# Kernel optimization log

Hardware: AMD Instinct MI355X
Metric: run time of the kernel (lower is better)

## Reference

```python
import jax, jax.numpy as jnp
import numpy as np

N2, N1, N0 = 25000, 50000, 100000
E2, E1, E0 = 250000, 500000, 1000000
CIN, H, COUT = 64, 128, 64
BN_EPS = 1e-5


def setup_inputs() -> dict:
    key = jax.random.key(0)
    ks = jax.random.split(key, 26)
    inp = {
        'x': jax.random.normal(ks[0], (N2, CIN), jnp.float32),
        'edge_index': jax.random.randint(ks[1], (2, E2), 0, N2),
        'xs0': jax.random.normal(ks[2], (N0, H), jnp.float32),
        'xs1': jax.random.normal(ks[3], (N1, H), jnp.float32),
        'ei0': jax.random.randint(ks[4], (2, E0), 0, N0),
        'ei1': jax.random.randint(ks[5], (2, E1), 0, N1),
        'ew0': jax.random.uniform(ks[6], (E0,), jnp.float32, 0.1, 1.0),
        'ew1': jax.random.uniform(ks[7], (E1,), jnp.float32, 0.1, 1.0),
        # pooling perms: unique indices of kept nodes at the finer level
        'perm0': jax.random.permutation(ks[8], N0)[:N1],
        'perm1': jax.random.permutation(ks[9], N1)[:N2],
        # GIN layer 1: in=64 -> hidden//2=64 (MLP: Lin, ReLU, Lin), then BN
        'W1a': 0.1 * jax.random.normal(ks[10], (CIN, H // 2), jnp.float32),
        'b1a': jnp.zeros((H // 2,), jnp.float32),
        'W1b': 0.1 * jax.random.normal(ks[11], (H // 2, H // 2), jnp.float32),
        'b1b': jnp.zeros((H // 2,), jnp.float32),
        'g1': jnp.ones((H // 2,), jnp.float32),
        'bt1': jnp.zeros((H // 2,), jnp.float32),
        # GIN layer 2: 64 -> hidden=128
        'W2a': 0.1 * jax.random.normal(ks[12], (H // 2, H), jnp.float32),
        'b2a': jnp.zeros((H,), jnp.float32),
        'W2b': 0.1 * jax.random.normal(ks[13], (H, H), jnp.float32),
        'b2b': jnp.zeros((H,), jnp.float32),
        'g2': jnp.ones((H,), jnp.float32),
        'bt2': jnp.zeros((H,), jnp.float32),
        # GCN up_convs (improved=True): hidden->hidden, hidden->out
        'Wg0': 0.1 * jax.random.normal(ks[14], (H, H), jnp.float32),
        'bg0': jnp.zeros((H,), jnp.float32),
        'Wg1': 0.1 * jax.random.normal(ks[15], (H, COUT), jnp.float32),
        'bg1': jnp.zeros((COUT,), jnp.float32),
    }
    return inp


def _gin_layer(x, ei, Wa, ba, Wb, bb, g, bt):
    """GINConv (eps=0) + ReLU + BatchNorm1d (training-mode stats)."""
    n = x.shape[0]
    agg = jax.ops.segment_sum(x[ei[0]], ei[1], num_segments=n)
    h = x + agg  # (1 + eps) * x + sum of neighbors, eps = 0
    h = jnp.maximum(h @ Wa + ba, 0.0) @ Wb + bb  # MLP: Lin-ReLU-Lin
    h = jnp.maximum(h, 0.0)  # F.relu on conv output
    mu = h.mean(axis=0)
    var = jnp.mean((h - mu) ** 2, axis=0)  # biased var (BatchNorm1d)
    return g * (h - mu) * jax.lax.rsqrt(var + BN_EPS) + bt


def _gcn_improved(x, ei, ew, W, b):
    """GCNConv(improved=True): self-loop weight 2, symmetric norm."""
    n = x.shape[0]
    h = x @ W
    deg = jax.ops.segment_sum(ew, ei[1], num_segments=n) + 2.0  # +2I self loops
    dis = jax.lax.rsqrt(deg)
    norm = dis[ei[0]] * ew * dis[ei[1]]
    out = jax.ops.segment_sum(norm[:, None] * h[ei[0]], ei[1], num_segments=n)
    out = out + (2.0 * dis * dis)[:, None] * h  # self-loop contribution
    return out + b


def reference(x, edge_index, xs0, xs1, ei0, ei1, ew0, ew1, perm0, perm1,
              W1a, b1a, W1b, b1b, g1, bt1,
              W2a, b2a, W2b, b2b, g2, bt2,
              Wg0, bg0, Wg1, bg1):
    # projection convs on the coarsest graph
    h = _gin_layer(x, edge_index, W1a, b1a, W1b, b1b, g1, bt1)
    h = _gin_layer(h, edge_index, W2a, b2a, W2b, b2b, g2, bt2)
    # upsample step 1 (i=0, j=1): scatter into level-1 graph, GCN, ReLU
    up = jnp.zeros_like(xs1).at[perm1].set(h)
    h = jnp.maximum(_gcn_improved(up, ei1, ew1, Wg0, bg0), 0.0)
    # upsample step 2 (i=1, j=0): scatter into level-0 graph, final GCN
    up = jnp.zeros_like(xs0).at[perm0].set(h)
    return _gcn_improved(up, ei0, ew0, Wg1, bg1)
```

## Files before the change

kernel.cpp:

```cpp
#include <hip/hip_runtime.h>
#include <hip/hip_fp16.h>
#include <type_traits>

#define NN2 25000
#define NN1 50000
#define NN0 100000
#define EE2 250000
#define EE1 500000
#define EE0 1000000
#define NTOTC 175000
#define ETOTC 1750000
#define NB 684
#define CHUNK 4096
#define NBLK 428
#define BN_EPS 1e-5f

static inline int cdiv(long a, long b) { return (int)((a + b - 1) / b); }

typedef _Float16 half8 __attribute__((ext_vector_type(8)));
typedef float f32x4 __attribute__((ext_vector_type(4)));

template <int K, int M, bool RELU, bool BNIN, bool BNOUT, typename OT>
__global__ __launch_bounds__(256) void mfma_gemm_kernel(
    const __half* __restrict__ in, const float* __restrict__ W,
    const float* __restrict__ bias,
    const float* __restrict__ sums, const float* __restrict__ sumsq,
    const float* __restrict__ g, const float* __restrict__ bt,
    float* __restrict__ osum, float* __restrict__ osq,
    OT* __restrict__ out, int n)
{
    constexpr int BM = 64;
    constexpr int LDA = K + 8;
    constexpr int NC = M / 16;
    __shared__ __align__(16) _Float16 Ah[BM * LDA];
    __shared__ __align__(16) _Float16 Wt[M * LDA];
    const int tid = threadIdx.x;
    const int r0 = blockIdx.x * BM;

    for (int idx = tid; idx < K * M; idx += 256) {
        int k = idx / M, m = idx % M;
        Wt[m * LDA + k] = (_Float16)W[idx];
    }
    for (int idx = tid; idx < BM * K; idx += 256) {
        int r = idx / K, k = idx % K;
        int gr = r0 + r;
        float v = (gr < n) ? __half2float(in[(long)gr * K + k]) : 0.f;
        if (BNIN) {
            float mu = sums[k] * (1.f / NN2);
            float rs = rsqrtf(sumsq[k] * (1.f / NN2) - mu * mu + BN_EPS);
            v = g[k] * rs * (v - mu) + bt[k];
        }
        Ah[r * LDA + k] = (_Float16)v;
    }
    __syncthreads();

    const int wid = tid >> 6, lane = tid & 63;
    const int rw = wid * 16;
    const int arow = rw + (lane & 15);
    const int koff = (lane >> 4) * 8;

    f32x4 acc[NC];
    #pragma unroll
    for (int c = 0; c < NC; ++c) acc[c] = f32x4{0.f, 0.f, 0.f, 0.f};

    #pragma unroll
    for (int k0 = 0; k0 < K; k0 += 32) {
        half8 a = *(const half8*)&Ah[arow * LDA + k0 + koff];
        #pragma unroll
        for (int c = 0; c < NC; ++c) {
            half8 b = *(const half8*)&Wt[(c * 16 + (lane & 15)) * LDA + k0 + koff];
            acc[c] = __builtin_amdgcn_mfma_f32_16x16x32_f16(a, b, acc[c], 0, 0, 0);
        }
    }

    float* bs = (float*)Ah;
    if (BNOUT) {
        __syncthreads();
        if (tid < 2 * M) bs[tid] = 0.f;
        __syncthreads();
    }

    const int drow = r0 + rw + 4 * (lane >> 4);
    #pragma unroll
    for (int c = 0; c < NC; ++c) {
        int col = c * 16 + (lane & 15);
        float bv = (bias != nullptr) ? bias[col] : 0.f;
        float sc = 0.f, qc = 0.f;
        #pragma unroll
        for (int j = 0; j < 4; ++j) {
            int r = drow + j;
            if (r < n) {
                float v = acc[c][j] + bv;
                if (RELU) v = fmaxf(v, 0.f);
                if constexpr (std::is_same<OT, __half>::value)
                    out[(long)r * M + col] = __float2half(v);
                else
                    out[(long)r * M + col] = v;
                if (BNOUT) { sc += v; qc += v * v; }
            }
        }
        if (BNOUT) {
            atomicAdd(&bs[col], sc);
            atomicAdd(&bs[M + col], qc);
        }
    }
    if (BNOUT) {
        __syncthreads();
        if (tid < M) {
            atomicAdd(&osum[tid], bs[tid]);
            atomicAdd(&osq[tid], bs[M + tid]);
        }
    }
}

__global__ void tohalf_kernel(const float* __restrict__ in, __half* __restrict__ out, int n4)
{
    int i = blockIdx.x * blockDim.x + threadIdx.x;
    if (i >= n4) return;
    float4 v = ((const float4*)in)[i];
    __half2 a = __floats2half2_rn(v.x, v.y);
    __half2 b = __floats2half2_rn(v.z, v.w);
    ((uint2*)out)[i] = make_uint2(*(unsigned*)&a, *(unsigned*)&b);
}

__global__ void translate_kernel(const int* __restrict__ src1, const int* __restrict__ src0,
                                 const int* __restrict__ inv1, const int* __restrict__ inv0,
                                 int* __restrict__ tcg)
{
    int e = blockIdx.x * blockDim.x + threadIdx.x;
    if (e < EE1) tcg[e] = inv1[src1[e]];
    else if (e < EE1 + EE0) tcg[e] = inv0[src0[e - EE1]];
}

__global__ __launch_bounds__(256) void count_kernel(
    const int* __restrict__ dst2, const int* __restrict__ dst1,
    const int* __restrict__ dst0, int* __restrict__ G)
{
    __shared__ int h[NB];
    int tid = threadIdx.x, blk = blockIdx.x;
    for (int i = tid; i < NB; i += 256) h[i] = 0;
    __syncthreads();
    int e0 = blk * CHUNK, e1 = min(e0 + CHUNK, ETOTC);
    for (int e = e0 + tid; e < e1; e += 256) {
        int vg;
        if (e < EE2) vg = dst2[e];
        else if (e < EE2 + EE1) vg = NN2 + dst1[e - EE2];
        else vg = NN2 + NN1 + dst0[e - EE2 - EE1];
        atomicAdd(&h[vg >> 8], 1);
    }
    __syncthreads();
    for (int i = tid; i < NB; i += 256) G[i * NBLK + blk] = h[i];
}

__global__ __launch_bounds__(256) void scan_block_kernel(int* data, int* bsum, int n)
{
    __shared__ int sh[256];
    int tid = threadIdx.x;
    int base = blockIdx.x * 1024 + tid * 4;
    int v[4];
    #pragma unroll
    for (int i = 0; i < 4; ++i) v[i] = (base + i < n) ? data[base + i] : 0;
    int tot = v[0] + v[1] + v[2] + v[3];
    sh[tid] = tot;
    __syncthreads();
    for (int d = 1; d < 256; d <<= 1) {
        int add = (tid >= d) ? sh[tid - d] : 0;
        __syncthreads();
        sh[tid] += add;
        __syncthreads();
    }
    int run = sh[tid] - tot;
    #pragma unroll
    for (int i = 0; i < 4; ++i) {
        if (base + i < n) data[base + i] = run;
        run += v[i];
    }
    if (tid == 255) bsum[blockIdx.x] = sh[255];
}

__global__ __launch_bounds__(512) void scan_bsum_kernel(int* bsum, int nb)
{
    __shared__ int sh[512];
    int tid = threadIdx.x;
    int v = (tid < nb) ? bsum[tid] : 0;
    sh[tid] = v;
    __syncthreads();
    for (int d = 1; d < 512; d <<= 1) {
        int add = (tid >= d) ? sh[tid - d] : 0;
        __syncthreads();
        sh[tid] += add;
        __syncthreads();
    }
    if (tid < nb) bsum[tid] = sh[tid] - v;
}

__global__ void scan_add_kernel(int* data, const int* __restrict__ bsum, int n)
{
    int i = blockIdx.x * blockDim.x + threadIdx.x;
    if (i < n) data[i] += bsum[i >> 10];
}

__global__ __launch_bounds__(256) void place_kernel(
    const int* __restrict__ src2, const int* __restrict__ dst2,
    const int* __restrict__ dst1, const float* __restrict__ ew1,
    const int* __restrict__ dst0, const float* __restrict__ ew0,
    const int* __restrict__ tcg,
    const int* __restrict__ G, int2* __restrict__ bedges)
{
    __shared__ int cur[NB];
    int tid = threadIdx.x, blk = blockIdx.x;
    for (int i = tid; i < NB; i += 256) cur[i] = G[i * NBLK + blk];
    __syncthreads();
    int e0 = blk * CHUNK, e1 = min(e0 + CHUNK, ETOTC);
    for (int e = e0 + tid; e < e1; e += 256) {
        int vg, c, ewb;
        if (e < EE2) {
            vg = dst2[e]; c = src2[e]; ewb = 0;
        } else if (e < EE2 + EE1) {
            int i = e - EE2;
            vg = NN2 + dst1[i]; c = tcg[i]; ewb = __float_as_int(ew1[i]);
        } else {
            int i = e - EE2 - EE1;
            vg = NN2 + NN1 + dst0[i]; c = tcg[EE1 + i]; ewb = __float_as_int(ew0[i]);
        }
        int b = vg >> 8, local = vg & 255;
        int pos = atomicAdd(&cur[b], 1);
        bedges[pos] = make_int2((local << 16) | (c + 1), ewb);
    }
}

__global__ __launch_bounds__(256) void bucket_build_kernel(
    const int2* __restrict__ bedges, const int* __restrict__ G,
    int* __restrict__ rp, int* __restrict__ re,
    int2* __restrict__ csr, float* __restrict__ dis)
{
    __shared__ int cnt[256];
    __shared__ float wdeg[256];
    __shared__ int excl[256];
    __shared__ int tsum[256];
    int b = blockIdx.x, tid = threadIdx.x;
    int s0 = G[b * NBLK];
    int s1 = (b == NB - 1) ? ETOTC : G[(b + 1) * NBLK];
    cnt[tid] = 0; wdeg[tid] = 0.f;
    __syncthreads();
    for (int i = s0 + tid; i < s1; i += 256) {
        int2 t = bedges[i];
        int local = t.x >> 16;
        atomicAdd(&wdeg[local], __int_as_float(t.y));
        if (t.x & 0xFFFF) atomicAdd(&cnt[local], 1);
    }
    __syncthreads();
    int v = cnt[tid];
    tsum[tid] = v;
    __syncthreads();
    for (int d = 1; d < 256; d <<= 1) {
        int add = (tid >= d) ? tsum[tid - d] : 0;
        __syncthreads();
        tsum[tid] += add;
        __syncthreads();
    }
    excl[tid] = tsum[tid] - v;
    {
        int vg = (b << 8) + tid;
        if (vg < NTOTC) {
            int r0_ = s0 + excl[tid];
            rp[vg] = r0_;
            re[vg] = r0_ + v;
            if (vg >= NN2) dis[vg - NN2] = rsqrtf(wdeg[tid] + 2.0f);
        }
    }
    cnt[tid] = 0;
    __syncthreads();
    for (int i = s0 + tid; i < s1; i += 256) {
        int2 t = bedges[i];
        int cx = t.x & 0xFFFF;
        if (cx) {
            int local = t.x >> 16;
            int pos = s0 + excl[local] + atomicAdd(&cnt[local], 1);
            csr[pos] = make_int2(cx - 1, t.y);
        }
    }
}

__global__ void inv_kernel(const int* __restrict__ perm1, const int* __restrict__ perm0,
                           int* __restrict__ inv1, int* __restrict__ inv0)
{
    int i = blockIdx.x * blockDim.x + threadIdx.x;
    if (i < NN2) inv1[perm1[i]] = i;
    else if (i < NN2 + NN1) inv0[perm0[i - NN2]] = i - NN2;
}

__global__ void disc_kernel(const int* __restrict__ perm1, const int* __restrict__ perm0,
                            const float* __restrict__ dis,
                            float* __restrict__ disc1, float* __restrict__ disc0)
{
    int i = blockIdx.x * blockDim.x + threadIdx.x;
    if (i < NN2) disc1[i] = dis[perm1[i]];
    else if (i < NN2 + NN1) disc0[i - NN2] = dis[NN1 + perm0[i - NN2]];
}

template <bool BN>
__global__ __launch_bounds__(256) void gin_gather_kernel(
    const __half* __restrict__ x, const int* __restrict__ rp, const int* __restrict__ re,
    const int2* __restrict__ csr,
    const float* __restrict__ sums, const float* __restrict__ sumsq,
    const float* __restrict__ g, const float* __restrict__ bt,
    __half* __restrict__ out, int n)
{
    int v = (blockIdx.x * 256 + threadIdx.x) >> 5;
    int lane = threadIdx.x & 31;
    if (v >= n) return;
    int p0 = rp[v], pe = re[v];
    float2 sv = __half22float2(*(const __half2*)(x + (long)v * 64 + lane * 2));
    float ax0 = sv.x, ay0 = sv.y;
    float ax1 = 0.f, ay1 = 0.f, ax2 = 0.f, ay2 = 0.f, ax3 = 0.f, ay3 = 0.f;
    for (int base = p0; base < pe; base += 32) {
        int idx = base + lane;
        int s_l = 0; float m_l = 0.f;
        if (idx < pe) { s_l = csr[idx].x; m_l = 1.f; }
        int cnt = min(32, pe - base);
        for (int j = 0; j < cnt; j += 4) {
            int s0 = __shfl(s_l, j, 32),     s1 = __shfl(s_l, j + 1, 32);
            int s2 = __shfl(s_l, j + 2, 32), s3 = __shfl(s_l, j + 3, 32);
            float m0 = __shfl(m_l, j, 32),     m1 = __shfl(m_l, j + 1, 32);
            float m2 = __shfl(m_l, j + 2, 32), m3 = __shfl(m_l, j + 3, 32);
            float2 h0 = __half22float2(*(const __half2*)(x + (long)s0 * 64 + lane * 2));
            float2 h1 = __half22float2(*(const __half2*)(x + (long)s1 * 64 + lane * 2));
            float2 h2 = __half22float2(*(const __half2*)(x + (long)s2 * 64 + lane * 2));
            float2 h3 = __half22float2(*(const __half2*)(x + (long)s3 * 64 + lane * 2));
            ax0 = fmaf(m0, h0.x, ax0); ay0 = fmaf(m0, h0.y, ay0);
            ax1 = fmaf(m1, h1.x, ax1); ay1 = fmaf(m1, h1.y, ay1);
            ax2 = fmaf(m2, h2.x, ax2); ay2 = fmaf(m2, h2.y, ay2);
            ax3 = fmaf(m3, h3.x, ax3); ay3 = fmaf(m3, h3.y, ay3);
        }
    }
    float accx = (ax0 + ax1) + (ax2 + ax3);
    float accy = (ay0 + ay1) + (ay2 + ay3);
    if (BN) {
        int deg = pe - p0;
        int c0 = lane * 2, c1 = lane * 2 + 1;
        float mu0 = sums[c0] * (1.f / NN2), mu1 = sums[c1] * (1.f / NN2);
        float rs0 = rsqrtf(sumsq[c0] * (1.f / NN2) - mu0 * mu0 + BN_EPS);
        float rs1 = rsqrtf(sumsq[c1] * (1.f / NN2) - mu1 * mu1 + BN_EPS);
        float a0 = g[c0] * rs0, a1 = g[c1] * rs1;
        accx = a0 * accx + (float)(deg + 1) * (bt[c0] - a0 * mu0);
        accy = a1 * accy + (float)(deg + 1) * (bt[c1] - a1 * mu1);
    }
    *(__half2*)(out + (long)v * 64 + lane * 2) = __floats2half2_rn(accx, accy);
}

template <bool RELU>
__global__ __launch_bounds__(256) void gcn_gather128_kernel(
    const __half* __restrict__ cmp, const int* __restrict__ inv,
    const int* __restrict__ rp, const int* __restrict__ re,
    const int2* __restrict__ csr, const float* __restrict__ disc,
    const float* __restrict__ dis, const float* __restrict__ bias,
    __half* __restrict__ out, int n)
{
    int v = (blockIdx.x * 256 + threadIdx.x) >> 5;
    int lane = threadIdx.x & 31;
    if (v >= n) return;
    int p0 = rp[v], pe = re[v];
    f32x4 a0 = {0,0,0,0}, a1 = {0,0,0,0}, a2 = {0,0,0,0}, a3 = {0,0,0,0};
    for (int base = p0; base < pe; base += 32) {
        int idx = base + lane;
        int cs_l = 0; float w_l = 0.f;
        if (idx < pe) {
            int2 sl = csr[idx];
            cs_l = sl.x;
            w_l = __int_as_float(sl.y) * disc[sl.x];
        }
        int cnt = min(32, pe - base);
        for (int j = 0; j < cnt; j += 4) {
            int c0 = __shfl(cs_l, j, 32),     c1 = __shfl(cs_l, j + 1, 32);
            int c2 = __shfl(cs_l, j + 2, 32), c3 = __shfl(cs_l, j + 3, 32);
            float w0 = __shfl(w_l, j, 32),     w1 = __shfl(w_l, j + 1, 32);
            float w2 = __shfl(w_l, j + 2, 32), w3 = __shfl(w_l, j + 3, 32);
            uint2 u0 = *(const uint2*)(cmp + (long)c0 * 128 + lane * 4);
            uint2 u1 = *(const uint2*)(cmp + (long)c1 * 128 + lane * 4);
            uint2 u2 = *(const uint2*)(cmp + (long)c2 * 128 + lane * 4);
            uint2 u3 = *(const uint2*)(cmp + (long)c3 * 128 + lane * 4);
            float2 p0a = __half22float2(*(__half2*)&u0.x), p0b = __half22float2(*(__half2*)&u0.y);
            float2 p1a = __half22float2(*(__half2*)&u1.x), p1b = __half22float2(*(__half2*)&u1.y);
            float2 p2a = __half22float2(*(__half2*)&u2.x), p2b = __half22float2(*(__half2*)&u2.y);
            float2 p3a = __half22float2(*(__half2*)&u3.x), p3b = __half22float2(*(__half2*)&u3.y);
            a0[0] = fmaf(w0, p0a.x, a0[0]); a0[1] = fmaf(w0, p0a.y, a0[1]);
            a0[2] = fmaf(w0, p0b.x, a0[2]); a0[3] = fmaf(w0, p0b.y, a0[3]);
            a1[0] = fmaf(w1, p1a.x, a1[0]); a1[1] = fmaf(w1, p1a.y, a1[1]);
            a1[2] = fmaf(w1, p1b.x, a1[2]); a1[3] = fmaf(w1, p1b.y, a1[3]);
            a2[0] = fmaf(w2, p2a.x, a2[0]); a2[1] = fmaf(w2, p2a.y, a2[1]);
            a2[2] = fmaf(w2, p2b.x, a2[2]); a2[3] = fmaf(w2, p2b.y, a2[3]);
            a3[0] = fmaf(w3, p3a.x, a3[0]); a3[1] = fmaf(w3, p3a.y, a3[1]);
            a3[2] = fmaf(w3, p3b.x, a3[2]); a3[3] = fmaf(w3, p3b.y, a3[3]);
        }
    }
    float dv = dis[v];
    int cv = inv[v];
    float sx0 = 0.f, sx1 = 0.f, sx2 = 0.f, sx3 = 0.f;
    if (cv >= 0) {
        uint2 u = *(const uint2*)(cmp + (long)cv * 128 + lane * 4);
        float2 pa = __half22float2(*(__half2*)&u.x), pb = __half22float2(*(__half2*)&u.y);
        sx0 = pa.x; sx1 = pa.y; sx2 = pb.x; sx3 = pb.y;
    }
    float s2 = 2.f * dv * dv;
    float o0 = fmaf(dv, (a0[0] + a1[0]) + (a2[0] + a3[0]), fmaf(s2, sx0, bias[lane * 4]));
    float o1 = fmaf(dv, (a0[1] + a1[1]) + (a2[1] + a3[1]), fmaf(s2, sx1, bias[lane * 4 + 1]));
    float o2 = fmaf(dv, (a0[2] + a1[2]) + (a2[2] + a3[2]), fmaf(s2, sx2, bias[lane * 4 + 2]));
    float o3 = fmaf(dv, (a0[3] + a1[3]) + (a2[3] + a3[3]), fmaf(s2, sx3, bias[lane * 4 + 3]));
    if (RELU) {
        o0 = fmaxf(o0, 0.f); o1 = fmaxf(o1, 0.f);
        o2 = fmaxf(o2, 0.f); o3 = fmaxf(o3, 0.f);
    }
    __half2 ha = __floats2half2_rn(o0, o1), hb = __floats2half2_rn(o2, o3);
    *(uint2*)(out + (long)v * 128 + lane * 4) = make_uint2(*(unsigned*)&ha, *(unsigned*)&hb);
}

template <bool RELU>
__global__ __launch_bounds__(256) void gcn_gather64_kernel(
    const __half* __restrict__ cmp, const int* __restrict__ inv,
    const int* __restrict__ rp, const int* __restrict__ re,
    const int2* __restrict__ csr, const float* __restrict__ disc,
    const float* __restrict__ dis, const float* __restrict__ bias,
    float* __restrict__ out, int n)
{
    int v = (blockIdx.x * 256 + threadIdx.x) >> 5;
    int lane = threadIdx.x & 31;
    if (v >= n) return;
    int p0 = rp[v], pe = re[v];
    float ax0 = 0.f, ay0 = 0.f, ax1 = 0.f, ay1 = 0.f;
    float ax2 = 0.f, ay2 = 0.f, ax3 = 0.f, ay3 = 0.f;
    for (int base = p0; base < pe; base += 32) {
        int idx = base + lane;
        int cs_l = 0; float w_l = 0.f;
        if (idx < pe) {
            int2 sl = csr[idx];
            cs_l = sl.x;
            w_l = __int_as_float(sl.y) * disc[sl.x];
        }
        int cnt = min(32, pe - base);
        for (int j = 0; j < cnt; j += 4) {
            int c0 = __shfl(cs_l, j, 32),     c1 = __shfl(cs_l, j + 1, 32);
            int c2 = __shfl(cs_l, j + 2, 32), c3 = __shfl(cs_l, j + 3, 32);
            float w0 = __shfl(w_l, j, 32),     w1 = __shfl(w_l, j + 1, 32);
            float w2 = __shfl(w_l, j + 2, 32), w3 = __shfl(w_l, j + 3, 32);
            float2 h0 = __half22float2(*(const __half2*)(cmp + (long)c0 * 64 + lane * 2));
            float2 h1 = __half22float2(*(const __half2*)(cmp + (long)c1 * 64 + lane * 2));
            float2 h2 = __half22float2(*(const __half2*)(cmp + (long)c2 * 64 + lane * 2));
            float2 h3 = __half22float2(*(const __half2*)(cmp + (long)c3 * 64 + lane * 2));
            ax0 = fmaf(w0, h0.x, ax0); ay0 = fmaf(w0, h0.y, ay0);
            ax1 = fmaf(w1, h1.x, ax1); ay1 = fmaf(w1, h1.y, ay1);
            ax2 = fmaf(w2, h2.x, ax2); ay2 = fmaf(w2, h2.y, ay2);
            ax3 = fmaf(w3, h3.x, ax3); ay3 = fmaf(w3, h3.y, ay3);
        }
    }
    float ax = (ax0 + ax1) + (ax2 + ax3);
    float ay = (ay0 + ay1) + (ay2 + ay3);
    float dv = dis[v];
    int cv = inv[v];
    float sx = 0.f, sy = 0.f;
    if (cv >= 0) {
        float2 hv = __half22float2(*(const __half2*)(cmp + (long)cv * 64 + lane * 2));
        sx = hv.x; sy = hv.y;
    }
    float s2 = 2.f * dv * dv;
    float o0 = fmaf(dv, ax, fmaf(s2, sx, bias[lane * 2]));
    float o1 = fmaf(dv, ay, fmaf(s2, sy, bias[lane * 2 + 1]));
    if (RELU) { o0 = fmaxf(o0, 0.f); o1 = fmaxf(o1, 0.f); }
    *(float2*)(out + (long)v * 64 + lane * 2) = make_float2(o0, o1);
}

extern "C" void kernel_launch(void* const* d_in, const int* in_sizes, int n_in,
                              void* d_out, int out_size, void* d_ws, size_t ws_size,
                              hipStream_t stream)
{
    const float* x    = (const float*)d_in[0];
    const int*   ei2  = (const int*)d_in[1];
    const int*   ei0  = (const int*)d_in[4];
    const int*   ei1  = (const int*)d_in[5];
    const float* ew0  = (const float*)d_in[6];
    const float* ew1  = (const float*)d_in[7];
    const int*   perm0= (const int*)d_in[8];
    const int*   perm1= (const int*)d_in[9];
    const float* W1a  = (const float*)d_in[10];
    const float* b1a  = (const float*)d_in[11];
    const float* W1b  = (const float*)d_in[12];
    const float* b1b  = (const float*)d_in[13];
    const float* g1   = (const float*)d_in[14];
    const float* bt1  = (const float*)d_in[15];
    const float* W2a  = (const float*)d_in[16];
    const float* b2a  = (const float*)d_in[17];
    const float* W2b  = (const float*)d_in[18];
    const float* b2b  = (const float*)d_in[19];
    const float* g2   = (const float*)d_in[20];
    const float* bt2  = (const float*)d_in[21];
    const float* Wg0  = (const float*)d_in[22];
    const float* bg0  = (const float*)d_in[23];
    const float* Wg1  = (const float*)d_in[24];
    const float* bg1  = (const float*)d_in[25];
    float* out = (float*)d_out;

    float* ws  = (float*)d_ws;
    int*   wsi = (int*)d_ws;

    int*   rp    = wsi;
    int*   re    = wsi + 176000;
    float* dis   = ws  + 352000;
    float* disc1 = ws  + 502000;
    float* disc0 = ws  + 527000;
    int*   inv1  = wsi + 577000;
    int*   inv0  = wsi + 627000;
    float* s1    = ws  + 727000;
    float* q1    = ws  + 727064;
    float* s2    = ws  + 727128;
    float* q2    = ws  + 727256;
    int*   bsum  = wsi + 727500;
    int*   G     = wsi + 728000;
    int2*  bedges= (int2*)(wsi + 1025000);
    int2*  csr   = (int2*)(wsi + 4525000);
    __half* xh   = (__half*)(wsi + 1025000);
    __half* t0f  = (__half*)(ws + 8025000);
    __half* BaF  = (__half*)(ws + 8825000);
    __half* t0h  = (__half*)(ws + 9625000);
    __half* t1   = (__half*)(ws + 10425000);
    __half* Ba   = (__half*)(ws + 11225000);
    __half* Bb   = (__half*)(ws + 12825000);
    __half* cmp1 = (__half*)(ws + 14425000);
    __half* out1 = (__half*)(ws + 16025000);
    __half* cmp0 = (__half*)(ws + 19225000);
    int*   tcg   = wsi + 20825000;

    const int* src2 = ei2, *dst2 = ei2 + EE2;
    const int* src1 = ei1, *dst1 = ei1 + EE1;
    const int* src0 = ei0, *dst0 = ei0 + EE0;

    const int NG = NB * NBLK;

    hipMemsetAsync(s1, 0, 384 * 4, stream);
    hipMemsetAsync(inv1, 0xFF, (NN1 + NN0) * 4, stream);
    inv_kernel<<<cdiv(NN2 + NN1, 256), 256, 0, stream>>>(perm1, perm0, inv1, inv0);
    translate_kernel<<<cdiv(EE1 + EE0, 256), 256, 0, stream>>>(src1, src0, inv1, inv0, tcg);
    count_kernel<<<NBLK, 256, 0, stream>>>(dst2, dst1, dst0, G);
    scan_block_kernel<<<cdiv(NG, 1024), 256, 0, stream>>>(G, bsum, NG);
    scan_bsum_kernel<<<1, 512, 0, stream>>>(bsum, cdiv(NG, 1024));
    scan_add_kernel<<<cdiv(NG, 256), 256, 0, stream>>>(G, bsum, NG);
    place_kernel<<<NBLK, 256, 0, stream>>>(
        src2, dst2, dst1, ew1, dst0, ew0, tcg, G, bedges);
    bucket_build_kernel<<<NB, 256, 0, stream>>>(bedges, G, rp, re, csr, dis);
    disc_kernel<<<cdiv(NN2 + NN1, 256), 256, 0, stream>>>(perm1, perm0, dis, disc1, disc0);
    tohalf_kernel<<<cdiv(NN2 * 16, 256), 256, 0, stream>>>(x, xh, NN2 * 16);

    gin_gather_kernel<false><<<cdiv((long)NN2 * 32, 256), 256, 0, stream>>>(
        xh, rp, re, csr, nullptr, nullptr, nullptr, nullptr, t0f, NN2);
    mfma_gemm_kernel<64, 64, true, false, false, __half><<<cdiv(NN2, 64), 256, 0, stream>>>(
        t0f, W1a, b1a, nullptr, nullptr, nullptr, nullptr, nullptr, nullptr, BaF, NN2);
    mfma_gemm_kernel<64, 64, true, false, true, __half><<<cdiv(NN2, 64), 256, 0, stream>>>(
        BaF, W1b, b1b, nullptr, nullptr, nullptr, nullptr, s1, q1, t0h, NN2);

    gin_gather_kernel<true><<<cdiv((long)NN2 * 32, 256), 256, 0, stream>>>(
        t0h, rp, re, csr, s1, q1, g1, bt1, t1, NN2);
    mfma_gemm_kernel<64, 128, true, false, false, __half><<<cdiv(NN2, 64), 256, 0, stream>>>(
        t1, W2a, b2a, nullptr, nullptr, nullptr, nullptr, nullptr, nullptr, Ba, NN2);
    mfma_gemm_kernel<128, 128, true, false, true, __half><<<cdiv(NN2, 64), 256, 0, stream>>>(
        Ba, W2b, b2b, nullptr, nullptr, nullptr, nullptr, s2, q2, Bb, NN2);

    mfma_gemm_kernel<128, 128, false, true, false, __half><<<cdiv(NN2, 64), 256, 0, stream>>>(
        Bb, Wg0, nullptr, s2, q2, g2, bt2, nullptr, nullptr, cmp1, NN2);
    gcn_gather128_kernel<true><<<cdiv((long)NN1 * 32, 256), 256, 0, stream>>>(
        cmp1, inv1, rp + NN2, re + NN2, csr, disc1, dis, bg0, out1, NN1);

    mfma_gemm_kernel<128, 64, false, false, false, __half><<<cdiv(NN1, 64), 256, 0, stream>>>(
        out1, Wg1, nullptr, nullptr, nullptr, nullptr, nullptr, nullptr, nullptr, cmp0, NN1);
    gcn_gather64_kernel<false><<<cdiv((long)NN0 * 32, 256), 256, 0, stream>>>(
        cmp0, inv0, rp + NN2 + NN1, re + NN2 + NN1, csr, disc0, dis + NN1, bg1, out, NN0);
}
```

Before: 265.6 us.

## Fuse GIN MLP GEMM pairs, merge translate into count, drop scan-add and memset

Fuses the two back-to-back MLP GEMMs of each GIN layer into one kernel that keeps the hidden activation in shared memory. It folds edge-source translation into the bucket count kernel and the BN-stat zeroing into inv_kernel. It drops the scan_add pass by adding block offsets where G is read, and halves the edge chunk size to double the block count. This removes several launches and an intermediate global round trip, at the cost of larger shared-memory use per block and a longer bsum scan.

```diff
diff --git a/kernel.cpp b/kernel.cpp
--- a/kernel.cpp
+++ b/kernel.cpp
@@ -11,8 +11,8 @@
 #define NTOTC 175000
 #define ETOTC 1750000
 #define NB 684
-#define CHUNK 4096
-#define NBLK 428
+#define CHUNK 2048
+#define NBLK 855
 #define BN_EPS 1e-5f
 
 static inline int cdiv(long a, long b) { return (int)((a + b - 1) / b); }
@@ -62,7 +62,6 @@
     f32x4 acc[NC];
     #pragma unroll
     for (int c = 0; c < NC; ++c) acc[c] = f32x4{0.f, 0.f, 0.f, 0.f};
-
     #pragma unroll
     for (int k0 = 0; k0 < K; k0 += 32) {
         half8 a = *(const half8*)&Ah[arow * LDA + k0 + koff];
@@ -79,7 +78,6 @@
         if (tid < 2 * M) bs[tid] = 0.f;
         __syncthreads();
     }
-
     const int drow = r0 + rw + 4 * (lane >> 4);
     #pragma unroll
     for (int c = 0; c < NC; ++c) {
@@ -99,17 +97,114 @@
                 if (BNOUT) { sc += v; qc += v * v; }
             }
         }
-        if (BNOUT) {
-            atomicAdd(&bs[col], sc);
-            atomicAdd(&bs[M + col], qc);
-        }
+        if (BNOUT) { atomicAdd(&bs[col], sc); atomicAdd(&bs[M + col], qc); }
     }
     if (BNOUT) {
         __syncthreads();
-        if (tid < M) {
-            atomicAdd(&osum[tid], bs[tid]);
-            atomicAdd(&osq[tid], bs[M + tid]);
-        }
+        if (tid < M) { atomicAdd(&osum[tid], bs[tid]); atomicAdd(&osq[tid], bs[M + tid]); }
+    }
+}
+
+template <int K, int M1, int M2, bool BNOUT>
+__global__ __launch_bounds__(256) void mlp_gemm_kernel(
+    const __half* __restrict__ in,
+    const float* __restrict__ W1, const float* __restrict__ b1,
+    const float* __restrict__ W2, const float* __restrict__ b2,
+    float* __restrict__ osum, float* __restrict__ osq,
+    __half* __restrict__ out, int n)
+{
+    constexpr int BM = 64;
+    constexpr int LDA = K + 8;
+    constexpr int LDM = M1 + 8;
+    constexpr int NC1 = M1 / 16, NC2 = M2 / 16;
+    __shared__ __align__(16) _Float16 Ah[BM * LDA];
+    __shared__ __align__(16) _Float16 Wt1[M1 * LDA];
+    __shared__ __align__(16) _Float16 Wt2[M2 * LDM];
+    __shared__ __align__(16) _Float16 mid[BM * LDM];
+    const int tid = threadIdx.x;
+    const int r0 = blockIdx.x * BM;
+
+    for (int idx = tid; idx < K * M1; idx += 256) {
+        int k = idx / M1, m = idx % M1;
+        Wt1[m * LDA + k] = (_Float16)W1[idx];
+    }
+    for (int idx = tid; idx < M1 * M2; idx += 256) {
+        int k = idx / M2, m = idx % M2;
+        Wt2[m * LDM + k] = (_Float16)W2[idx];
+    }
+    for (int idx = tid; idx < BM * K; idx += 256) {
+        int r = idx / K, k = idx % K;
+        int gr = r0 + r;
+        Ah[r * LDA + k] = (gr < n) ? (_Float16)in[(long)gr * K + k] : (_Float16)0.f;
+    }
+    __syncthreads();
+
+    const int wid = tid >> 6, lane = tid & 63;
+    const int rw = wid * 16;
+    const int arow = rw + (lane & 15);
+    const int koff = (lane >> 4) * 8;
+
+    f32x4 acc1[NC1];
+    #pragma unroll
+    for (int c = 0; c < NC1; ++c) acc1[c] = f32x4{0.f, 0.f, 0.f, 0.f};
+    #pragma unroll
+    for (int k0 = 0; k0 < K; k0 += 32) {
+        half8 a = *(const half8*)&Ah[arow * LDA + k0 + koff];
+        #pragma unroll
+        for (int c = 0; c < NC1; ++c) {
+            half8 b = *(const half8*)&Wt1[(c * 16 + (lane & 15)) * LDA + k0 + koff];
+            acc1[c] = __builtin_amdgcn_mfma_f32_16x16x32_f16(a, b, acc1[c], 0, 0, 0);
+        }
+    }
+    {
+        int rd0 = rw + 4 * (lane >> 4);
+        #pragma unroll
+        for (int c = 0; c < NC1; ++c) {
+            int col = c * 16 + (lane & 15);
+            float bv = b1[col];
+            #pragma unroll
+            for (int j = 0; j < 4; ++j)
+                mid[(rd0 + j) * LDM + col] = (_Float16)fmaxf(acc1[c][j] + bv, 0.f);
+        }
+    }
+    float* bs = (float*)Ah;
+    if (BNOUT) {
+        if (tid < 2 * M2) bs[tid] = 0.f;
+    }
+    __syncthreads();
+
+    f32x4 acc2[NC2];
+    #pragma unroll
+    for (int c = 0; c < NC2; ++c) acc2[c] = f32x4{0.f, 0.f, 0.f, 0.f};
+    #pragma unroll
+    for (int k0 = 0; k0 < M1; k0 += 32) {
+        half8 a = *(const half8*)&mid[arow * LDM + k0 + koff];
+        #pragma unroll
+        for (int c = 0; c < NC2; ++c) {
+            half8 b = *(const half8*)&Wt2[(c * 16 + (lane & 15)) * LDM + k0 + koff];
+            acc2[c] = __builtin_amdgcn_mfma_f32_16x16x32_f16(a, b, acc2[c], 0, 0, 0);
+        }
+    }
+    const int drow = r0 + rw + 4 * (lane >> 4);
+    #pragma unroll
+    for (int c = 0; c < NC2; ++c) {
+        int col = c * 16 + (lane & 15);
+        float bv = b2[col];
+        float sc = 0.f, qc = 0.f;
+        #pragma unroll
+        for (int j = 0; j < 4; ++j) {
+            int r = drow + j;
+            if (r < n) {
+                float v = fmaxf(acc2[c][j] + bv, 0.f);
+                out[(long)r * M2 + col] = __float2half(v);
+                if (BNOUT) { sc += v; qc += v * v; }
+            }
+        }
+        if (BNOUT) { atomicAdd(&bs[col], sc); atomicAdd(&bs[M2 + col], qc); }
+    }
+    if (BNOUT) {
+        __syncthreads();
+        if (tid < M2) { atomicAdd(&osum[tid], bs[tid]); atomicAdd(&osq[tid], bs[M2 + tid]); }
     }
 }
 
@@ -123,18 +218,12 @@
     ((uint2*)out)[i] = make_uint2(*(unsigned*)&a, *(unsigned*)&b);
 }
 
-__global__ void translate_kernel(const int* __restrict__ src1, const int* __restrict__ src0,
-                                 const int* __restrict__ inv1, const int* __restrict__ inv0,
-                                 int* __restrict__ tcg)
-{
-    int e = blockIdx.x * blockDim.x + threadIdx.x;
-    if (e < EE1) tcg[e] = inv1[src1[e]];
-    else if (e < EE1 + EE0) tcg[e] = inv0[src0[e - EE1]];
-}
-
-__global__ __launch_bounds__(256) void count_kernel(
-    const int* __restrict__ dst2, const int* __restrict__ dst1,
-    const int* __restrict__ dst0, int* __restrict__ G)
+__global__ __launch_bounds__(256) void count_translate_kernel(
+    const int* __restrict__ dst2,
+    const int* __restrict__ src1, const int* __restrict__ dst1,
+    const int* __restrict__ src0, const int* __restrict__ dst0,
+    const int* __restrict__ inv1, const int* __restrict__ inv0,
+    int* __restrict__ tcg, int* __restrict__ G)
 {
     __shared__ int h[NB];
     int tid = threadIdx.x, blk = blockIdx.x;
@@ -143,9 +232,17 @@
     int e0 = blk * CHUNK, e1 = min(e0 + CHUNK, ETOTC);
     for (int e = e0 + tid; e < e1; e += 256) {
         int vg;
-        if (e < EE2) vg = dst2[e];
-        else if (e < EE2 + EE1) vg = NN2 + dst1[e - EE2];
-        else vg = NN2 + NN1 + dst0[e - EE2 - EE1];
+        if (e < EE2) {
+            vg = dst2[e];
+        } else if (e < EE2 + EE1) {
+            int i = e - EE2;
+            vg = NN2 + dst1[i];
+            tcg[i] = inv1[src1[i]];
+        } else {
+            int i = e - EE2 - EE1;
+            vg = NN2 + NN1 + dst0[i];
+            tcg[EE1 + i] = inv0[src0[i]];
+        }
         atomicAdd(&h[vg >> 8], 1);
     }
     __syncthreads();
@@ -178,26 +275,20 @@
     if (tid == 255) bsum[blockIdx.x] = sh[255];
 }
 
-__global__ __launch_bounds__(512) void scan_bsum_kernel(int* bsum, int nb)
-{
-    __shared__ int sh[512];
+__global__ __launch_bounds__(1024) void scan_bsum_kernel(int* bsum, int nb)
+{
+    __shared__ int sh[1024];
     int tid = threadIdx.x;
     int v = (tid < nb) ? bsum[tid] : 0;
     sh[tid] = v;
     __syncthreads();
-    for (int d = 1; d < 512; d <<= 1) {
+    for (int d = 1; d < 1024; d <<= 1) {
         int add = (tid >= d) ? sh[tid - d] : 0;
         __syncthreads();
         sh[tid] += add;
         __syncthreads();
     }
     if (tid < nb) bsum[tid] = sh[tid] - v;
-}
-
-__global__ void scan_add_kernel(int* data, const int* __restrict__ bsum, int n)
-{
-    int i = blockIdx.x * blockDim.x + threadIdx.x;
-    if (i < n) data[i] += bsum[i >> 10];
 }
 
 __global__ __launch_bounds__(256) void place_kernel(
@@ -205,11 +296,15 @@
     const int* __restrict__ dst1, const float* __restrict__ ew1,
     const int* __restrict__ dst0, const float* __restrict__ ew0,
     const int* __restrict__ tcg,
-    const int* __restrict__ G, int2* __restrict__ bedges)
+    const int* __restrict__ G, const int* __restrict__ bsum,
+    int2* __restrict__ bedges)
 {
     __shared__ int cur[NB];
     int tid = threadIdx.x, blk = blockIdx.x;
-    for (int i = tid; i < NB; i += 256) cur[i] = G[i * NBLK + blk];
+    for (int i = tid; i < NB; i += 256) {
+        int idx = i * NBLK + blk;
+        cur[i] = G[idx] + bsum[idx >> 10];
+    }
     __syncthreads();
     int e0 = blk * CHUNK, e1 = min(e0 + CHUNK, ETOTC);
     for (int e = e0 + tid; e < e1; e += 256) {
@@ -231,6 +326,7 @@
 
 __global__ __launch_bounds__(256) void bucket_build_kernel(
     const int2* __restrict__ bedges, const int* __restrict__ G,
+    const int* __restrict__ bsum,
     int* __restrict__ rp, int* __restrict__ re,
     int2* __restrict__ csr, float* __restrict__ dis)
 {
@@ -239,8 +335,11 @@
     __shared__ int excl[256];
     __shared__ int tsum[256];
     int b = blockIdx.x, tid = threadIdx.x;
-    int s0 = G[b * NBLK];
-    int s1 = (b == NB - 1) ? ETOTC : G[(b + 1) * NBLK];
+    int i0 = b * NBLK;
+    int s0 = G[i0] + bsum[i0 >> 10];
+    int s1;
+    if (b == NB - 1) s1 = ETOTC;
+    else { int i1 = (b + 1) * NBLK; s1 = G[i1] + bsum[i1 >> 10]; }
     cnt[tid] = 0; wdeg[tid] = 0.f;
     __syncthreads();
     for (int i = s0 + tid; i < s1; i += 256) {
@@ -283,9 +382,11 @@
 }
 
 __global__ void inv_kernel(const int* __restrict__ perm1, const int* __restrict__ perm0,
-                           int* __restrict__ inv1, int* __restrict__ inv0)
+                           int* __restrict__ inv1, int* __restrict__ inv0,
+                           float* __restrict__ bnz)
 {
     int i = blockIdx.x * blockDim.x + threadIdx.x;
+    if (i < 384) bnz[i] = 0.f;
     if (i < NN2) inv1[perm1[i]] = i;
     else if (i < NN2 + NN1) inv0[perm0[i - NN2]] = i - NN2;
 }
@@ -514,20 +615,18 @@
     float* s2    = ws  + 727128;
     float* q2    = ws  + 727256;
     int*   bsum  = wsi + 727500;
-    int*   G     = wsi + 728000;
-    int2*  bedges= (int2*)(wsi + 1025000);
-    int2*  csr   = (int2*)(wsi + 4525000);
-    __half* xh   = (__half*)(wsi + 1025000);
-    __half* t0f  = (__half*)(ws + 8025000);
-    __half* BaF  = (__half*)(ws + 8825000);
-    __half* t0h  = (__half*)(ws + 9625000);
-    __half* t1   = (__half*)(ws + 10425000);
-    __half* Ba   = (__half*)(ws + 11225000);
-    __half* Bb   = (__half*)(ws + 12825000);
-    __half* cmp1 = (__half*)(ws + 14425000);
-    __half* out1 = (__half*)(ws + 16025000);
-    __half* cmp0 = (__half*)(ws + 19225000);
-    int*   tcg   = wsi + 20825000;
+    int*   G     = wsi + 729000;
+    int2*  bedges= (int2*)(wsi + 1315000);
+    int2*  csr   = (int2*)(wsi + 4815000);
+    __half* xh   = (__half*)(wsi + 1315000);
+    __half* t0f  = (__half*)(ws + 8315000);
+    __half* t0h  = (__half*)(ws + 9115000);
+    __half* t1   = (__half*)(ws + 9915000);
+    __half* Bb   = (__half*)(ws + 10715000);
+    __half* cmp1 = (__half*)(ws + 12315000);
+    __half* out1 = (__half*)(ws + 13915000);
+    __half* cmp0 = (__half*)(ws + 17115000);
+    int*   tcg   = wsi + 18715000;
 
     const int* src2 = ei2, *dst2 = ei2 + EE2;
     const int* src1 = ei1, *dst1 = ei1 + EE1;
@@ -535,33 +634,27 @@
 
     const int NG = NB * NBLK;
 
-    hipMemsetAsync(s1, 0, 384 * 4, stream);
     hipMemsetAsync(inv1, 0xFF, (NN1 + NN0) * 4, stream);
-    inv_kernel<<<cdiv(NN2 + NN1, 256), 256, 0, stream>>>(perm1, perm0, inv1, inv0);
-    translate_kernel<<<cdiv(EE1 + EE0, 256), 256, 0, stream>>>(src1, src0, inv1, inv0, tcg);
-    count_kernel<<<NBLK, 256, 0, stream>>>(dst2, dst1, dst0, G);
+    inv_kernel<<<cdiv(NN2 + NN1, 256), 256, 0, stream>>>(perm1, perm0, inv1, inv0, s1);
+    count_translate_kernel<<<NBLK, 256, 0, stream>>>(
+        dst2, src1, dst1, src0, dst0, inv1, inv0, tcg, G);
     scan_block_kernel<<<cdiv(NG, 1024), 256, 0, stream>>>(G, bsum, NG);
-    scan_bsum_kernel<<<1, 512, 0, stream>>>(bsum, cdiv(NG, 1024));
-    scan_add_kernel<<<cdiv(NG, 256), 256, 0, stream>>>(G, bsum, NG);
+    scan_bsum_kernel<<<1, 1024, 0, stream>>>(bsum, cdiv(NG, 1024));
     place_kernel<<<NBLK, 256, 0, stream>>>(
-        src2, dst2, dst1, ew1, dst0, ew0, tcg, G, bedges);
-    bucket_build_kernel<<<NB, 256, 0, stream>>>(bedges, G, rp, re, csr, dis);
+        src2, dst2, dst1, ew1, dst0, ew0, tcg, G, bsum, bedges);
+    bucket_build_kernel<<<NB, 256, 0, stream>>>(bedges, G, bsum, rp, re, csr, dis);
     disc_kernel<<<cdiv(NN2 + NN1, 256), 256, 0, stream>>>(perm1, perm0, dis, disc1, disc0);
     tohalf_kernel<<<cdiv(NN2 * 16, 256), 256, 0, stream>>>(x, xh, NN2 * 16);
 
     gin_gather_kernel<false><<<cdiv((long)NN2 * 32, 256), 256, 0, stream>>>(
         xh, rp, re, csr, nullptr, nullptr, nullptr, nullptr, t0f, NN2);
-    mfma_gemm_kernel<64, 64, true, false, false, __half><<<cdiv(NN2, 64), 256, 0, stream>>>(
-        t0f, W1a, b1a, nullptr, nullptr, nullptr, nullptr, nullptr, nullptr, BaF, NN2);
-    mfma_gemm_kernel<64, 64, true, false, true, __half><<<cdiv(NN2, 64), 256, 0, stream>>>(
-        BaF, W1b, b1b, nullptr, nullptr, nullptr, nullptr, s1, q1, t0h, NN2);
+    mlp_gemm_kernel<64, 64, 64, true><<<cdiv(NN2, 64), 256, 0, stream>>>(
+        t0f, W1a, b1a, W1b, b1b, s1, q1, t0h, NN2);
 
     gin_gather_kernel<true><<<cdiv((long)NN2 * 32, 256), 256, 0, stream>>>(
         t0h, rp, re, csr, s1, q1, g1, bt1, t1, NN2);
-    mfma_gemm_kernel<64, 128, true, false, false, __half><<<cdiv(NN2, 64), 256, 0, stream>>>(
-        t1, W2a, b2a, nullptr, nullptr, nullptr, nullptr, nullptr, nullptr, Ba, NN2);
-    mfma_gemm_kernel<128, 128, true, false, true, __half><<<cdiv(NN2, 64), 256, 0, stream>>>(
-        Ba, W2b, b2b, nullptr, nullptr, nullptr, nullptr, s2, q2, Bb, NN2);
+    mlp_gemm_kernel<64, 128, 128, true><<<cdiv(NN2, 64), 256, 0, stream>>>(
+        t1, W2a, b2a, W2b, b2b, s2, q2, Bb, NN2);
 
     mfma_gemm_kernel<128, 128, false, true, false, __half><<<cdiv(NN2, 64), 256, 0, stream>>>(
         Bb, Wg0, nullptr, s2, q2, g2, bt2, nullptr, nullptr, cmp1, NN2);
```

New measurement: 237.1 us. -10.7%, faster.
